# Kernel optimization log

Measured on AMD Instinct MI355X. Metric: run time of the kernel, lower is better.

## Reference

```python
import jax, jax.numpy as jnp
import numpy as np

N = 20000   # nodes
E = 320000  # edges
H = 4       # attention heads
GAT_SLOPE = 0.2   # DGL GATv2Conv internal leaky_relu slope
ACT_SLOPE = 0.01  # nn.LeakyReLU default slope


def gatv2_layer(h, src, dst, Wl, Wr, attn, b):
    """DGL GATv2Conv (share_weights=False, bias=True, eval mode).
    h: [N, Fin]; Wl/Wr: [Fin, H*D]; attn: [H, D]; b: [H*D]. Returns [N, H, D]."""
    n = h.shape[0]
    Hh, D = attn.shape
    fs = (h @ Wl).reshape(n, Hh, D)  # source projection
    fd = (h @ Wr).reshape(n, Hh, D)  # destination projection
    # edge-wise GATv2 score: a^T leaky_relu(Wl h_u + Wr h_v)
    e = jax.nn.leaky_relu(fs[src] + fd[dst], negative_slope=GAT_SLOPE)  # [E,H,D]
    logit = jnp.einsum('ehd,hd->eh', e, attn)  # [E,H]
    # edge softmax over incoming edges of each dst node (numerically stable)
    m = jax.ops.segment_max(logit, dst, num_segments=n)
    a = jnp.exp(logit - m[dst])
    s = jax.ops.segment_sum(a, dst, num_segments=n)
    alpha = a / s[dst]  # [E,H]
    out = jax.ops.segment_sum(alpha[:, :, None] * fs[src], dst, num_segments=n)
    return out + b.reshape(1, Hh, D)


def setup_inputs() -> dict:
    key = jax.random.key(0)
    ks = jax.random.split(key, 16)

    def w(k, shape, fan_in):
        return (jax.random.normal(k, shape, jnp.float32) / np.float32(np.sqrt(fan_in)))

    return {
        'n_feat': jax.random.normal(ks[0], (N, 512), jnp.float32),
        'src': jax.random.randint(ks[1], (E,), 0, N, jnp.int32),
        'dst': jax.random.randint(ks[2], (E,), 0, N, jnp.int32),
        # layer 0: 512 -> H x 128
        'Wl0': w(ks[3], (512, H * 128), 512), 'Wr0': w(ks[4], (512, H * 128), 512),
        'attn0': w(ks[5], (H, 128), 128), 'b0': jnp.zeros((H * 128,), jnp.float32),
        # layer 1: 128 -> H x 128
        'Wl1': w(ks[6], (128, H * 128), 128), 'Wr1': w(ks[7], (128, H * 128), 128),
        'attn1': w(ks[8], (H, 128), 128), 'b1': jnp.zeros((H * 128,), jnp.float32),
        # layer 2 (output): 128 -> H x 64
        'Wl2': w(ks[9], (128, H * 64), 128), 'Wr2': w(ks[10], (128, H * 64), 128),
        'attn2': w(ks[11], (H, 64), 64), 'b2': jnp.zeros((H * 64,), jnp.float32),
    }


def reference(n_feat, src, dst, Wl0, Wr0, attn0, b0, Wl1, Wr1, attn1, b1,
              Wl2, Wr2, attn2, b2):
    h = n_feat.reshape(n_feat.shape[0], -1)  # nn.Flatten
    for (Wl, Wr, attn, b) in ((Wl0, Wr0, attn0, b0),
                              (Wl1, Wr1, attn1, b1),
                              (Wl2, Wr2, attn2, b2)):
        h = gatv2_layer(h, src, dst, Wl, Wr, attn, b)  # [N,H,D]
        h = h.mean(axis=1)                              # head mean
        h = jax.nn.leaky_relu(h, negative_slope=ACT_SLOPE)
    # dgl.mean_nodes: per-graph mean readout (single graph -> [1, out])
    return h.mean(axis=0, keepdims=True)
```

## Files before the change

kernel.cpp:

```cpp
#include <hip/hip_runtime.h>
#include <hip/hip_bf16.h>
#include <stdint.h>


#define GAT_SLOPE 0.2f
#define ACT_SLOPE 0.01f
#define MAXDEG 64

typedef _Float16 half8 __attribute__((ext_vector_type(8)));
typedef _Float16 v2h __attribute__((ext_vector_type(2)));
typedef float floatx4 __attribute__((ext_vector_type(4)));

struct TransDesc {
  const float* src;
  _Float16* dst;
  int K, M, off;
};
struct PreArgs {
  TransDesc d[6];
  int wTotal;
  const float* nf;
  _Float16* A0;
  int aTotal;
  const int* src;
  const int* dst;
  int* counts;
  int* pcsrc;
  int E;
};

__global__ __launch_bounds__(256) void preproc_kernel(PreArgs pa) {
  int i = blockIdx.x * 256 + threadIdx.x;
  const int total = pa.wTotal + pa.aTotal + pa.E;
  if (i >= total) return;
  if (i < pa.wTotal) {
    int q = 0;
#pragma unroll
    for (int j = 1; j < 6; ++j)
      if (i >= pa.d[j].off) q = j;
    int local = i - pa.d[q].off;
    int K = pa.d[q].K, M = pa.d[q].M;
    int m = local / K, k = local % K;
    pa.d[q].dst[local] = (_Float16)pa.d[q].src[(size_t)k * M + m];
  } else if (i < pa.wTotal + pa.aTotal) {
    int j = i - pa.wTotal;
    pa.A0[j] = (_Float16)pa.nf[j];
  } else {
    int e = i - pa.wTotal - pa.aTotal;
    int d = pa.dst[e];
    int pos = atomicAdd(&pa.counts[d], 1);
    if (pos < MAXDEG) pa.pcsrc[(size_t)d * MAXDEG + pos] = pa.src[e];
  }
}

__device__ __forceinline__ void gload_lds16(const _Float16* g, _Float16* l) {
  __builtin_amdgcn_global_load_lds(
      (__attribute__((address_space(1))) unsigned int*)g,
      (__attribute__((address_space(3))) unsigned int*)l, 16, 0, 0);
}

#define TM 128
#define TN 128
#define TK 32

__global__ __launch_bounds__(256) void gemm_mfma_dual_kernel(
    const _Float16* __restrict__ A, const _Float16* __restrict__ B0,
    const _Float16* __restrict__ B1, _Float16* __restrict__ C0,
    _Float16* __restrict__ C1, int Nrow, int K, int M, int nStrips,
    int nbxLog2) {
  const int id = blockIdx.x;
  const int xcd = id & 7;
  const int s = id >> 3;
  const int nbx = 1 << nbxLog2;
  const int col = s & (nbx - 1);
  const int chunk = s >> nbxLog2;
  const int strip = chunk * 8 + xcd;
  if (strip >= nStrips) return;

  const int nb = nbx >> 1;
  const bool second = col >= nb;
  const _Float16* B = second ? B1 : B0;
  _Float16* C = second ? C1 : C0;
  const int bn = (second ? col - nb : col) * TN;
  const int bm = strip * TM;

  __shared__ __align__(16) _Float16 As[TM * TK];
  __shared__ __align__(16) _Float16 Bs[TN * TK];

  const int tid = threadIdx.x;
  const int w = tid >> 6;
  const int lane = tid & 63;
  const int wr = w >> 1;
  const int wc = w & 1;
  const int quad = lane >> 4;
  const int lr = lane & 15;

  const int lrow = lane >> 2;
  const int loff = (lane & 3) * 8;

  floatx4 acc[4][4];
#pragma unroll
  for (int i = 0; i < 4; ++i)
#pragma unroll
    for (int j = 0; j < 4; ++j) acc[i][j] = (floatx4){0.f, 0.f, 0.f, 0.f};

  const int KT = K / TK;
  for (int kt = 0; kt < KT; ++kt) {
    const int k0 = kt * TK;
#pragma unroll
    for (int half = 0; half < 2; ++half) {
      const int r0 = w * 32 + half * 16;
      int ga = bm + r0 + lrow;
      if (ga >= Nrow) ga = Nrow - 1;
      gload_lds16(A + (size_t)ga * K + k0 + loff, As + r0 * TK);
      gload_lds16(B + (size_t)(bn + r0 + lrow) * K + k0 + loff, Bs + r0 * TK);
    }
    __syncthreads();

    half8 ar[4], br[4];
#pragma unroll
    for (int i = 0; i < 4; ++i) {
      int row = wr * 64 + i * 16 + lr;
      ar[i] = *(const half8*)(As + row * TK + quad * 8);
    }
#pragma unroll
    for (int j = 0; j < 4; ++j) {
      int colr = wc * 64 + j * 16 + lr;
      br[j] = *(const half8*)(Bs + colr * TK + quad * 8);
    }
#pragma unroll
    for (int i = 0; i < 4; ++i)
#pragma unroll
      for (int j = 0; j < 4; ++j)
        acc[i][j] = __builtin_amdgcn_mfma_f32_16x16x32_f16(ar[i], br[j],
                                                           acc[i][j], 0, 0, 0);
    __syncthreads();
  }

#pragma unroll
  for (int i = 0; i < 4; ++i) {
#pragma unroll
    for (int r = 0; r < 4; ++r) {
      int row = bm + wr * 64 + i * 16 + quad * 4 + r;
      if (row >= Nrow) continue;
#pragma unroll
      for (int j = 0; j < 4; ++j) {
        int colc = bn + wc * 64 + j * 16 + lr;
        C[(size_t)row * M + colc] = (_Float16)acc[i][j][r];
      }
    }
  }
}

template <int D>
__global__ __launch_bounds__(128) void node_attn_kernel(
    const _Float16* __restrict__ fs, const _Float16* __restrict__ fd,
    const int* __restrict__ counts, const int* __restrict__ pcsrc,
    const float* __restrict__ attn, const float* __restrict__ bias,
    float* __restrict__ hout, _Float16* __restrict__ oh, int N) {
  constexpr int HD = 4 * D;
  constexpr int R = HD / 64;
  constexpr int R2 = R / 2;
  typedef _Float16 halfR __attribute__((ext_vector_type(R)));
  union Frag {
    halfR v;
    v2h h[R2];
    _Float16 s[R];
  };
  const int v = blockIdx.x;
  if (v >= N) return;
  const int wid = threadIdx.x >> 6;
  const int lane = threadIdx.x & 63;

  const v2h slope2 = {(_Float16)GAT_SLOPE, (_Float16)GAT_SLOPE};

  Frag fdv;
  fdv.v = *(const halfR*)(fd + (size_t)v * HD + lane * R);
  v2h ar2[R2];
#pragma unroll
  for (int j = 0; j < R2; ++j) {
    ar2[j][0] = (_Float16)attn[lane * R + 2 * j];
    ar2[j][1] = (_Float16)attn[lane * R + 2 * j + 1];
  }

  float m = -INFINITY, l = 0.f;
  float O[R];
#pragma unroll
  for (int i = 0; i < R; ++i) O[i] = 0.f;

  const int cnt = min(counts[v], MAXDEG);
  const int* elist = pcsrc + (size_t)v * MAXDEG;
  const int mid = (cnt + 1) >> 1;
  int k = wid ? mid : 0;
  const int ke = wid ? cnt : mid;

  for (; k + 3 < ke; k += 4) {
    const int s0 = elist[k];
    const int s1 = elist[k + 1];
    const int s2 = elist[k + 2];
    const int s3 = elist[k + 3];
    Frag t0, t1, t2, t3;
    t0.v = *(const halfR*)(fs + (size_t)s0 * HD + lane * R);
    t1.v = *(const halfR*)(fs + (size_t)s1 * HD + lane * R);
    t2.v = *(const halfR*)(fs + (size_t)s2 * HD + lane * R);
    t3.v = *(const halfR*)(fs + (size_t)s3 * HD + lane * R);
    float p0 = 0.f, p1 = 0.f, p2 = 0.f, p3 = 0.f;
#pragma unroll
    for (int j = 0; j < R2; ++j) {
      v2h x0 = t0.h[j] + fdv.h[j];
      v2h x1 = t1.h[j] + fdv.h[j];
      v2h x2 = t2.h[j] + fdv.h[j];
      v2h x3 = t3.h[j] + fdv.h[j];
      x0 = __builtin_elementwise_max(x0, x0 * slope2);
      x1 = __builtin_elementwise_max(x1, x1 * slope2);
      x2 = __builtin_elementwise_max(x2, x2 * slope2);
      x3 = __builtin_elementwise_max(x3, x3 * slope2);
      p0 = __builtin_amdgcn_fdot2(ar2[j], x0, p0, false);
      p1 = __builtin_amdgcn_fdot2(ar2[j], x1, p1, false);
      p2 = __builtin_amdgcn_fdot2(ar2[j], x2, p2, false);
      p3 = __builtin_amdgcn_fdot2(ar2[j], x3, p3, false);
    }
#pragma unroll
    for (int off = 1; off <= 8; off <<= 1) {
      p0 += __shfl_xor(p0, off, 64);
      p1 += __shfl_xor(p1, off, 64);
      p2 += __shfl_xor(p2, off, 64);
      p3 += __shfl_xor(p3, off, 64);
    }
    const float mq = fmaxf(fmaxf(p0, p1), fmaxf(p2, p3));
    const float w0 = __expf(p0 - mq);
    const float w1 = __expf(p1 - mq);
    const float w2 = __expf(p2 - mq);
    const float w3 = __expf(p3 - mq);
    const float mnew = fmaxf(m, mq);
    const float sc = __expf(m - mnew);
    const float sq = __expf(mq - mnew);
    l = l * sc + (w0 + w1 + w2 + w3) * sq;
#pragma unroll
    for (int i = 0; i < R; ++i) {
      float acc = (float)t0.s[i] * w0;
      acc = fmaf((float)t1.s[i], w1, acc);
      acc = fmaf((float)t2.s[i], w2, acc);
      acc = fmaf((float)t3.s[i], w3, acc);
      O[i] = fmaf(O[i], sc, sq * acc);
    }
    m = mnew;
  }
  for (; k < ke; ++k) {
    const int s0 = elist[k];
    Frag t0;
    t0.v = *(const halfR*)(fs + (size_t)s0 * HD + lane * R);
    float p0 = 0.f;
#pragma unroll
    for (int j = 0; j < R2; ++j) {
      v2h x0 = t0.h[j] + fdv.h[j];
      x0 = __builtin_elementwise_max(x0, x0 * slope2);
      p0 = __builtin_amdgcn_fdot2(ar2[j], x0, p0, false);
    }
#pragma unroll
    for (int off = 1; off <= 8; off <<= 1) p0 += __shfl_xor(p0, off, 64);
    const float mnew = fmaxf(m, p0);
    const float sc = __expf(m - mnew);
    const float p = __expf(p0 - mnew);
    l = l * sc + p;
#pragma unroll
    for (int i = 0; i < R; ++i) O[i] = fmaf(O[i], sc, p * (float)t0.s[i]);
    m = mnew;
  }

  __shared__ float sO[64 * R];
  __shared__ float sM[64];
  __shared__ float sL[64];
  if (wid == 1) {
    sM[lane] = m;
    sL[lane] = l;
#pragma unroll
    for (int i = 0; i < R; ++i) sO[lane * R + i] = O[i];
  }
  __syncthreads();
  if (wid == 1) return;
  {
    const float m1 = sM[lane];
    const float l1 = sL[lane];
    const float mstar = fmaxf(m, m1);
    const float a0 = (l > 0.f) ? __expf(m - mstar) : 0.f;
    const float a1 = (l1 > 0.f) ? __expf(m1 - mstar) : 0.f;
    l = l * a0 + l1 * a1;
#pragma unroll
    for (int i = 0; i < R; ++i) O[i] = O[i] * a0 + sO[lane * R + i] * a1;
  }

  const float inv = (l > 0.f) ? 1.f / l : 0.f;
#pragma unroll
  for (int i = 0; i < R; ++i) O[i] = O[i] * inv + bias[lane * R + i];
#pragma unroll
  for (int i = 0; i < R; ++i) {
    O[i] += __shfl_xor(O[i], 16, 64);
    O[i] += __shfl_xor(O[i], 32, 64);
    float x = O[i] * 0.25f;
    O[i] = x > 0.f ? x : x * ACT_SLOPE;
  }
  if (lane < 16) {
    const size_t base = (size_t)v * D + lane * R;
    if (hout) {
#pragma unroll
      for (int i = 0; i < R; ++i) hout[base + i] = O[i];
    }
    if (oh) {
#pragma unroll
      for (int i = 0; i < R; ++i) oh[base + i] = (_Float16)O[i];
    }
  }
}

__global__ __launch_bounds__(64) void final_mean_kernel(
    const float* __restrict__ h, float* __restrict__ out, int N) {
  const int d = threadIdx.x;
  float acc = 0.f;
  for (int n = blockIdx.x; n < N; n += gridDim.x) acc += h[(size_t)n * 64 + d];
  atomicAdd(&out[d], acc / (float)N);
}

extern "C" void kernel_launch(void* const* d_in, const int* in_sizes, int n_in,
                              void* d_out, int out_size, void* d_ws,
                              size_t ws_size, hipStream_t stream) {
  const float* n_feat = (const float*)d_in[0];
  const int* src = (const int*)d_in[1];
  const int* dst = (const int*)d_in[2];
  const float* Wl[3] = {(const float*)d_in[3], (const float*)d_in[7],
                        (const float*)d_in[11]};
  const float* Wr[3] = {(const float*)d_in[4], (const float*)d_in[8],
                        (const float*)d_in[12]};
  const float* attn[3] = {(const float*)d_in[5], (const float*)d_in[9],
                          (const float*)d_in[13]};
  const float* bias[3] = {(const float*)d_in[6], (const float*)d_in[10],
                          (const float*)d_in[14]};

  const int N = in_sizes[0] / 512;
  const int E = in_sizes[1];
  const int Kdim[3] = {512, 128, 128};
  const int Mdim[3] = {512, 512, 256};

  char* ws = (char*)d_ws;
  size_t o = 0;
  auto alloc = [&](size_t bytes) {
    void* p = ws + o;
    o += (bytes + 15) & ~(size_t)15;
    return p;
  };
  _Float16* fs = (_Float16*)alloc((size_t)N * 512 * 2);
  _Float16* fd = (_Float16*)alloc((size_t)N * 512 * 2);
  _Float16* A0 = (_Float16*)alloc((size_t)N * 512 * 2);
  _Float16* h1 = (_Float16*)alloc((size_t)N * 128 * 2);
  _Float16* h2 = (_Float16*)alloc((size_t)N * 128 * 2);
  float* hfin = (float*)alloc((size_t)N * 64 * 4);
  _Float16 *WlT[3], *WrT[3];
  for (int L = 0; L < 3; ++L) {
    size_t sz = (size_t)Kdim[L] * Mdim[L] * 2;
    WlT[L] = (_Float16*)alloc(sz);
    WrT[L] = (_Float16*)alloc(sz);
  }
  int* counts = (int*)alloc((size_t)N * 4);
  int* pcsrc = (int*)alloc((size_t)N * MAXDEG * 4);

  hipMemsetAsync(counts, 0, (size_t)N * sizeof(int), stream);
  {
    PreArgs pa;
    int off = 0;
    for (int L = 0; L < 3; ++L) {
      pa.d[2 * L] = {Wl[L], WlT[L], Kdim[L], Mdim[L], off};
      off += Kdim[L] * Mdim[L];
      pa.d[2 * L + 1] = {Wr[L], WrT[L], Kdim[L], Mdim[L], off};
      off += Kdim[L] * Mdim[L];
    }
    pa.wTotal = off;
    pa.nf = n_feat;
    pa.A0 = A0;
    pa.aTotal = N * 512;
    pa.src = src;
    pa.dst = dst;
    pa.counts = counts;
    pa.pcsrc = pcsrc;
    pa.E = E;
    int total = pa.wTotal + pa.aTotal + pa.E;
    preproc_kernel<<<(total + 255) / 256, 256, 0, stream>>>(pa);
  }

  const _Float16* Ain[3] = {A0, h1, h2};

  const int nStrips = (N + TM - 1) / TM;
  const int S8 = ((nStrips + 7) / 8) * 8;

  for (int L = 0; L < 3; ++L) {
    const int K = Kdim[L], M = Mdim[L];
    const int nbx = 2 * M / TN;
    const int nbxLog2 = (nbx == 8) ? 3 : 2;
    gemm_mfma_dual_kernel<<<S8 * nbx, 256, 0, stream>>>(
        Ain[L], WlT[L], WrT[L], fs, fd, N, K, M, nStrips, nbxLog2);
    if (L == 0) {
      node_attn_kernel<128><<<N, 128, 0, stream>>>(fs, fd, counts, pcsrc,
                                                   attn[L], bias[L], nullptr,
                                                   h1, N);
    } else if (L == 1) {
      node_attn_kernel<128><<<N, 128, 0, stream>>>(fs, fd, counts, pcsrc,
                                                   attn[L], bias[L], nullptr,
                                                   h2, N);
    } else {
      node_attn_kernel<64><<<N, 128, 0, stream>>>(fs, fd, counts, pcsrc,
                                                  attn[L], bias[L], hfin,
                                                  nullptr, N);
    }
  }

  hipMemsetAsync(d_out, 0, 64 * sizeof(float), stream);
  final_mean_kernel<<<256, 64, 0, stream>>>(hfin, (float*)d_out, N);
}
```

Before: 356.5 us.

## Process one node per wavefront with batched, double-buffered neighbor gathers

The attention kernel now assigns one wavefront per destination node, four nodes per 256-thread block, instead of splitting each node's edges across two waves and merging them through shared memory. The neighbor index list is loaded into one register per lane and broadcast with readlane. Source-feature rows are gathered eight at a time into two alternating register buffers, so the next batch's loads overlap with the current batch's online-softmax math. Head reductions use DPP row adds instead of shuffles, and the attention vector is pre-converted to fp16 in the preprocessing kernel. The cost is much higher register pressure from 16 in-flight fragments, plus padded loads of the last neighbor for partial batches.

```diff
diff --git a/kernel.cpp b/kernel.cpp
--- a/kernel.cpp
+++ b/kernel.cpp
@@ -17,7 +17,7 @@
   int K, M, off;
 };
 struct PreArgs {
-  TransDesc d[6];
+  TransDesc d[9];
   int wTotal;
   const float* nf;
   _Float16* A0;
@@ -36,7 +36,7 @@
   if (i < pa.wTotal) {
     int q = 0;
 #pragma unroll
-    for (int j = 1; j < 6; ++j)
+    for (int j = 1; j < 9; ++j)
       if (i >= pa.d[j].off) q = j;
     int local = i - pa.d[q].off;
     int K = pa.d[q].K, M = pa.d[q].M;
@@ -152,11 +152,25 @@
   }
 }
 
+template <int CTRL>
+__device__ __forceinline__ float dpp_add(float x) {
+  int y = __builtin_amdgcn_update_dpp(0, __builtin_bit_cast(int, x), CTRL,
+                                      0xF, 0xF, true);
+  return x + __builtin_bit_cast(float, y);
+}
+__device__ __forceinline__ float row_sum16(float x) {
+  x = dpp_add<0x121>(x);
+  x = dpp_add<0x122>(x);
+  x = dpp_add<0x124>(x);
+  x = dpp_add<0x128>(x);
+  return x;
+}
+
 template <int D>
-__global__ __launch_bounds__(128) void node_attn_kernel(
+__global__ __launch_bounds__(256) void node_attn_kernel(
     const _Float16* __restrict__ fs, const _Float16* __restrict__ fd,
     const int* __restrict__ counts, const int* __restrict__ pcsrc,
-    const float* __restrict__ attn, const float* __restrict__ bias,
+    const _Float16* __restrict__ attnT, const float* __restrict__ bias,
     float* __restrict__ hout, _Float16* __restrict__ oh, int N) {
   constexpr int HD = 4 * D;
   constexpr int R = HD / 64;
@@ -167,127 +181,88 @@
     v2h h[R2];
     _Float16 s[R];
   };
-  const int v = blockIdx.x;
-  if (v >= N) return;
   const int wid = threadIdx.x >> 6;
   const int lane = threadIdx.x & 63;
+  const int v = blockIdx.x * 4 + wid;
+  if (v >= N) return;
 
   const v2h slope2 = {(_Float16)GAT_SLOPE, (_Float16)GAT_SLOPE};
 
+  const int cnt = min(counts[v], MAXDEG);
+  int idxReg = pcsrc[(size_t)v * MAXDEG + lane];
   Frag fdv;
   fdv.v = *(const halfR*)(fd + (size_t)v * HD + lane * R);
-  v2h ar2[R2];
-#pragma unroll
-  for (int j = 0; j < R2; ++j) {
-    ar2[j][0] = (_Float16)attn[lane * R + 2 * j];
-    ar2[j][1] = (_Float16)attn[lane * R + 2 * j + 1];
-  }
+  Frag arf;
+  arf.v = *(const halfR*)(attnT + lane * R);
 
   float m = -INFINITY, l = 0.f;
   float O[R];
 #pragma unroll
   for (int i = 0; i < R; ++i) O[i] = 0.f;
 
-  const int cnt = min(counts[v], MAXDEG);
-  const int* elist = pcsrc + (size_t)v * MAXDEG;
-  const int mid = (cnt + 1) >> 1;
-  int k = wid ? mid : 0;
-  const int ke = wid ? cnt : mid;
-
-  for (; k + 3 < ke; k += 4) {
-    const int s0 = elist[k];
-    const int s1 = elist[k + 1];
-    const int s2 = elist[k + 2];
-    const int s3 = elist[k + 3];
-    Frag t0, t1, t2, t3;
-    t0.v = *(const halfR*)(fs + (size_t)s0 * HD + lane * R);
-    t1.v = *(const halfR*)(fs + (size_t)s1 * HD + lane * R);
-    t2.v = *(const halfR*)(fs + (size_t)s2 * HD + lane * R);
-    t3.v = *(const halfR*)(fs + (size_t)s3 * HD + lane * R);
-    float p0 = 0.f, p1 = 0.f, p2 = 0.f, p3 = 0.f;
-#pragma unroll
-    for (int j = 0; j < R2; ++j) {
-      v2h x0 = t0.h[j] + fdv.h[j];
-      v2h x1 = t1.h[j] + fdv.h[j];
-      v2h x2 = t2.h[j] + fdv.h[j];
-      v2h x3 = t3.h[j] + fdv.h[j];
-      x0 = __builtin_elementwise_max(x0, x0 * slope2);
-      x1 = __builtin_elementwise_max(x1, x1 * slope2);
-      x2 = __builtin_elementwise_max(x2, x2 * slope2);
-      x3 = __builtin_elementwise_max(x3, x3 * slope2);
-      p0 = __builtin_amdgcn_fdot2(ar2[j], x0, p0, false);
-      p1 = __builtin_amdgcn_fdot2(ar2[j], x1, p1, false);
-      p2 = __builtin_amdgcn_fdot2(ar2[j], x2, p2, false);
-      p3 = __builtin_amdgcn_fdot2(ar2[j], x3, p3, false);
-    }
-#pragma unroll
-    for (int off = 1; off <= 8; off <<= 1) {
-      p0 += __shfl_xor(p0, off, 64);
-      p1 += __shfl_xor(p1, off, 64);
-      p2 += __shfl_xor(p2, off, 64);
-      p3 += __shfl_xor(p3, off, 64);
-    }
-    const float mq = fmaxf(fmaxf(p0, p1), fmaxf(p2, p3));
-    const float w0 = __expf(p0 - mq);
-    const float w1 = __expf(p1 - mq);
-    const float w2 = __expf(p2 - mq);
-    const float w3 = __expf(p3 - mq);
-    const float mnew = fmaxf(m, mq);
-    const float sc = __expf(m - mnew);
-    const float sq = __expf(mq - mnew);
-    l = l * sc + (w0 + w1 + w2 + w3) * sq;
-#pragma unroll
-    for (int i = 0; i < R; ++i) {
-      float acc = (float)t0.s[i] * w0;
-      acc = fmaf((float)t1.s[i], w1, acc);
-      acc = fmaf((float)t2.s[i], w2, acc);
-      acc = fmaf((float)t3.s[i], w3, acc);
-      O[i] = fmaf(O[i], sc, sq * acc);
-    }
-    m = mnew;
-  }
-  for (; k < ke; ++k) {
-    const int s0 = elist[k];
-    Frag t0;
-    t0.v = *(const halfR*)(fs + (size_t)s0 * HD + lane * R);
-    float p0 = 0.f;
-#pragma unroll
-    for (int j = 0; j < R2; ++j) {
-      v2h x0 = t0.h[j] + fdv.h[j];
-      x0 = __builtin_elementwise_max(x0, x0 * slope2);
-      p0 = __builtin_amdgcn_fdot2(ar2[j], x0, p0, false);
-    }
-#pragma unroll
-    for (int off = 1; off <= 8; off <<= 1) p0 += __shfl_xor(p0, off, 64);
-    const float mnew = fmaxf(m, p0);
-    const float sc = __expf(m - mnew);
-    const float p = __expf(p0 - mnew);
-    l = l * sc + p;
-#pragma unroll
-    for (int i = 0; i < R; ++i) O[i] = fmaf(O[i], sc, p * (float)t0.s[i]);
-    m = mnew;
-  }
-
-  __shared__ float sO[64 * R];
-  __shared__ float sM[64];
-  __shared__ float sL[64];
-  if (wid == 1) {
-    sM[lane] = m;
-    sL[lane] = l;
-#pragma unroll
-    for (int i = 0; i < R; ++i) sO[lane * R + i] = O[i];
-  }
-  __syncthreads();
-  if (wid == 1) return;
-  {
-    const float m1 = sM[lane];
-    const float l1 = sL[lane];
-    const float mstar = fmaxf(m, m1);
-    const float a0 = (l > 0.f) ? __expf(m - mstar) : 0.f;
-    const float a1 = (l1 > 0.f) ? __expf(m1 - mstar) : 0.f;
-    l = l * a0 + l1 * a1;
-#pragma unroll
-    for (int i = 0; i < R; ++i) O[i] = O[i] * a0 + sO[lane * R + i] * a1;
+  if (cnt > 0) {
+    const int lastIdx = __builtin_amdgcn_readlane(idxReg, cnt - 1);
+    const int nb = (cnt + 7) >> 3;
+
+    auto loadb = [&](Frag* t, int base) {
+#pragma unroll
+      for (int q = 0; q < 8; ++q) {
+        const int bq = base + q;
+        const int sidx =
+            (bq < cnt) ? __builtin_amdgcn_readlane(idxReg, bq) : lastIdx;
+        t[q].v = *(const halfR*)(fs + (size_t)sidx * HD + lane * R);
+      }
+    };
+
+    auto compute = [&](Frag* t, int base) {
+      float p[8];
+#pragma unroll
+      for (int q = 0; q < 8; ++q) {
+        float acc = 0.f;
+#pragma unroll
+        for (int j = 0; j < R2; ++j) {
+          v2h x = t[q].h[j] + fdv.h[j];
+          x = __builtin_elementwise_max(x, x * slope2);
+          acc = __builtin_amdgcn_fdot2(arf.h[j], x, acc, false);
+        }
+        acc = row_sum16(acc);
+        p[q] = (base + q < cnt) ? acc : -INFINITY;
+      }
+      float mnew = m;
+#pragma unroll
+      for (int q = 0; q < 8; ++q) mnew = fmaxf(mnew, p[q]);
+      const float sc = __expf(m - mnew);
+      float w[8];
+      float wsum = 0.f;
+#pragma unroll
+      for (int q = 0; q < 8; ++q) {
+        w[q] = __expf(p[q] - mnew);
+        wsum += w[q];
+      }
+      l = l * sc + wsum;
+#pragma unroll
+      for (int i = 0; i < R; ++i) {
+        float acc = (float)t[0].s[i] * w[0];
+#pragma unroll
+        for (int q = 1; q < 8; ++q) acc = fmaf((float)t[q].s[i], w[q], acc);
+        O[i] = fmaf(O[i], sc, acc);
+      }
+      m = mnew;
+    };
+
+    Frag tA[8], tB[8];
+    loadb(tA, 0);
+    int bi = 0;
+    for (;;) {
+      if (bi + 1 < nb) loadb(tB, (bi + 1) * 8);
+      compute(tA, bi * 8);
+      ++bi;
+      if (bi == nb) break;
+      if (bi + 1 < nb) loadb(tA, (bi + 1) * 8);
+      compute(tB, bi * 8);
+      ++bi;
+      if (bi == nb) break;
+    }
   }
 
   const float inv = (l > 0.f) ? 1.f / l : 0.f;
@@ -340,6 +315,7 @@
   const int E = in_sizes[1];
   const int Kdim[3] = {512, 128, 128};
   const int Mdim[3] = {512, 512, 256};
+  const int attnLen[3] = {512, 512, 256};
 
   char* ws = (char*)d_ws;
   size_t o = 0;
@@ -354,12 +330,13 @@
   _Float16* h1 = (_Float16*)alloc((size_t)N * 128 * 2);
   _Float16* h2 = (_Float16*)alloc((size_t)N * 128 * 2);
   float* hfin = (float*)alloc((size_t)N * 64 * 4);
-  _Float16 *WlT[3], *WrT[3];
+  _Float16 *WlT[3], *WrT[3], *attnT[3];
   for (int L = 0; L < 3; ++L) {
     size_t sz = (size_t)Kdim[L] * Mdim[L] * 2;
     WlT[L] = (_Float16*)alloc(sz);
     WrT[L] = (_Float16*)alloc(sz);
   }
+  for (int L = 0; L < 3; ++L) attnT[L] = (_Float16*)alloc(attnLen[L] * 2);
   int* counts = (int*)alloc((size_t)N * 4);
   int* pcsrc = (int*)alloc((size_t)N * MAXDEG * 4);
 
@@ -372,6 +349,10 @@
       off += Kdim[L] * Mdim[L];
       pa.d[2 * L + 1] = {Wr[L], WrT[L], Kdim[L], Mdim[L], off};
       off += Kdim[L] * Mdim[L];
+    }
+    for (int L = 0; L < 3; ++L) {
+      pa.d[6 + L] = {attn[L], attnT[L], attnLen[L], 1, off};
+      off += attnLen[L];
     }
     pa.wTotal = off;
     pa.nf = n_feat;
@@ -391,6 +372,8 @@
   const int nStrips = (N + TM - 1) / TM;
   const int S8 = ((nStrips + 7) / 8) * 8;
 
+  const int attnGrid = (N + 3) / 4;
+
   for (int L = 0; L < 3; ++L) {
     const int K = Kdim[L], M = Mdim[L];
     const int nbx = 2 * M / TN;
@@ -398,17 +381,14 @@
     gemm_mfma_dual_kernel<<<S8 * nbx, 256, 0, stream>>>(
         Ain[L], WlT[L], WrT[L], fs, fd, N, K, M, nStrips, nbxLog2);
     if (L == 0) {
-      node_attn_kernel<128><<<N, 128, 0, stream>>>(fs, fd, counts, pcsrc,
-                                                   attn[L], bias[L], nullptr,
-                                                   h1, N);
+      node_attn_kernel<128><<<attnGrid, 256, 0, stream>>>(
+          fs, fd, counts, pcsrc, attnT[L], bias[L], nullptr, h1, N);
     } else if (L == 1) {
-      node_attn_kernel<128><<<N, 128, 0, stream>>>(fs, fd, counts, pcsrc,
-                                                   attn[L], bias[L], nullptr,
-                                                   h2, N);
+      node_attn_kernel<128><<<attnGrid, 256, 0, stream>>>(
+          fs, fd, counts, pcsrc, attnT[L], bias[L], nullptr, h2, N);
     } else {
-      node_attn_kernel<64><<<N, 128, 0, stream>>>(fs, fd, counts, pcsrc,
-                                                  attn[L], bias[L], hfin,
-                                                  nullptr, N);
+      node_attn_kernel<64><<<attnGrid, 256, 0, stream>>>(
+          fs, fd, counts, pcsrc, attnT[L], bias[L], hfin, nullptr, N);
     }
   }
 
```

Measured after the change: 353.4 us. No clear change (-0.9%).
